# Optimization experiments

Hardware: AMD Instinct MI355X
Metric: run time of the kernel (lower is better)

Reference implementation:

```python
import math
import jax, jax.numpy as jnp
import numpy as np

D_MODEL = 1024
N_HEAD = 16
HEAD_DIM = D_MODEL // N_HEAD
BS, SEQ = 2, 2048


def setup_inputs() -> dict:
    key = jax.random.key(0)
    ks = jax.random.split(key, 10)
    s = 1.0 / math.sqrt(D_MODEL)  # ~torch Linear init scale
    x = jax.random.normal(ks[0], (BS, SEQ, D_MODEL), dtype=jnp.float32)
    bias = jax.random.normal(ks[1], (1, N_HEAD, SEQ, SEQ), dtype=jnp.float32)
    mask = jax.random.randint(ks[2], (1, 1, SEQ, SEQ), 0, 2, dtype=jnp.int32)
    wq = jax.random.uniform(ks[3], (D_MODEL, D_MODEL), jnp.float32, -s, s)
    bq = jax.random.uniform(ks[4], (D_MODEL,), jnp.float32, -s, s)
    wk = jax.random.uniform(ks[5], (D_MODEL, D_MODEL), jnp.float32, -s, s)
    bk = jax.random.uniform(ks[6], (D_MODEL,), jnp.float32, -s, s)
    wv = jax.random.uniform(ks[7], (D_MODEL, D_MODEL), jnp.float32, -s, s)
    bv = jax.random.uniform(ks[8], (D_MODEL,), jnp.float32, -s, s)
    return {"x": x, "bias": bias, "mask": mask,
            "wq": wq, "bq": bq, "wk": wk, "bk": bk, "wv": wv, "bv": bv}


def _split_heads(t):
    bs, s, _ = t.shape
    return t.reshape(bs, s, N_HEAD, HEAD_DIM).transpose(0, 2, 1, 3)  # [b,h,s,d]


def reference(x, bias, mask, wq, bq, wk, bk, wv, bv):
    # torch Linear: y = x @ W^T + b
    q = _split_heads(x @ wq.T + bq)
    k = _split_heads(x @ wk.T + bk)
    v = _split_heads(x @ wv.T + bv)
    scale = 1.0 / math.sqrt(HEAD_DIM)
    logits = jnp.einsum('bhqd,bhkd->bhqk', q, k) * scale + bias  # [b,h,S,S]
    logits = jnp.where(mask == 0, jnp.float32(-1e9), logits)
    atten_weights = jax.nn.softmax(logits, axis=-1)
    output = jnp.einsum('bhqk,bhkd->bhqd', atten_weights, v)  # [b,h,S,hd]
    return (output, atten_weights)
```

## Files before the change

### kernel.cpp

```cpp
#include <hip/hip_runtime.h>

typedef __attribute__((ext_vector_type(8))) short bf16x8;
typedef __attribute__((ext_vector_type(4))) float f32x4;
typedef __attribute__((ext_vector_type(4))) int i32x4;
typedef __attribute__((ext_vector_type(4))) unsigned short us4;

#define N_HEAD 16
#define SEQ 2048

__device__ __forceinline__ unsigned short f2bf(float f) {
  union { float f; unsigned u; } v; v.f = f;
  unsigned r = v.u + 0x7fffu + ((v.u >> 16) & 1u);
  return (unsigned short)(r >> 16);
}

__global__ void conv_bf16(const float* __restrict__ x,
                          const float* __restrict__ wq,
                          const float* __restrict__ wk,
                          const float* __restrict__ wv,
                          unsigned short* __restrict__ xb,
                          unsigned short* __restrict__ wb)
{
  size_t i = ((size_t)blockIdx.x * 256 + threadIdx.x) * 8;
  const float* src;
  unsigned short* dst;
  size_t off;
  if (i < 4194304) { src = x; dst = xb; off = i; }
  else {
    size_t j = i - 4194304;
    int w = (int)(j >> 20);
    off = j & 1048575u;
    src = (w == 0) ? wq : (w == 1) ? wk : wv;
    dst = wb + ((size_t)w << 20);
  }
  float4 a = *(const float4*)(src + off);
  float4 b = *(const float4*)(src + off + 4);
  us4 u0 = { f2bf(a.x), f2bf(a.y), f2bf(a.z), f2bf(a.w) };
  us4 u1 = { f2bf(b.x), f2bf(b.y), f2bf(b.z), f2bf(b.w) };
  *(us4*)(dst + off) = u0;
  *(us4*)(dst + off + 4) = u1;
}

__global__ __launch_bounds__(256, 2)
void qkv_gemm_bf16(const unsigned short* __restrict__ xb,
                   const unsigned short* __restrict__ wb,
                   const float* __restrict__ bq, const float* __restrict__ bk,
                   const float* __restrict__ bv,
                   unsigned short* __restrict__ qws,
                   unsigned short* __restrict__ kws,
                   unsigned short* __restrict__ vtws)
{
  __shared__ unsigned short As[128 * 40];
  __shared__ unsigned short Bs[128 * 40];

  const int tid  = threadIdx.x;
  const int wave = tid >> 6, lane = tid & 63;
  const int quad = lane >> 4, lrow = lane & 15;
  const int wm = wave >> 1, wn = wave & 1;
  const int m0 = blockIdx.x * 128, n0 = blockIdx.y * 128;
  const int z = blockIdx.z;

  const unsigned short* W = wb + ((size_t)z << 20);
  const float* bvec = (z == 0) ? bq : (z == 1) ? bk : bv;

  f32x4 acc[4][4];
  #pragma unroll
  for (int mi = 0; mi < 4; ++mi)
    #pragma unroll
    for (int ni = 0; ni < 4; ++ni)
      acc[mi][ni] = (f32x4){0.f, 0.f, 0.f, 0.f};

  const int srow = tid >> 1, scol = (tid & 1) * 16;
  const unsigned short* xsrc = xb + (size_t)(m0 + srow) * 1024 + scol;
  const unsigned short* wsrc = W  + (size_t)(n0 + srow) * 1024 + scol;

  bf16x8 va0 = *(const bf16x8*)(xsrc);
  bf16x8 va1 = *(const bf16x8*)(xsrc + 8);
  bf16x8 vb0 = *(const bf16x8*)(wsrc);
  bf16x8 vb1 = *(const bf16x8*)(wsrc + 8);

  for (int k0 = 0; k0 < 1024; k0 += 32) {
    __syncthreads();
    *(bf16x8*)&As[srow * 40 + scol]     = va0;
    *(bf16x8*)&As[srow * 40 + scol + 8] = va1;
    *(bf16x8*)&Bs[srow * 40 + scol]     = vb0;
    *(bf16x8*)&Bs[srow * 40 + scol + 8] = vb1;
    __syncthreads();
    if (k0 < 992) {
      va0 = *(const bf16x8*)(xsrc + k0 + 32);
      va1 = *(const bf16x8*)(xsrc + k0 + 40);
      vb0 = *(const bf16x8*)(wsrc + k0 + 32);
      vb1 = *(const bf16x8*)(wsrc + k0 + 40);
    }
    bf16x8 a[4], b[4];
    #pragma unroll
    for (int mi = 0; mi < 4; ++mi)
      a[mi] = *(const bf16x8*)&As[(wm * 64 + mi * 16 + lrow) * 40 + quad * 8];
    #pragma unroll
    for (int ni = 0; ni < 4; ++ni)
      b[ni] = *(const bf16x8*)&Bs[(wn * 64 + ni * 16 + lrow) * 40 + quad * 8];
    #pragma unroll
    for (int mi = 0; mi < 4; ++mi)
      #pragma unroll
      for (int ni = 0; ni < 4; ++ni)
        acc[mi][ni] = __builtin_amdgcn_mfma_f32_16x16x32_bf16(a[mi], b[ni], acc[mi][ni], 0, 0, 0);
  }

  float badd[4];
  #pragma unroll
  for (int ni = 0; ni < 4; ++ni) badd[ni] = bvec[n0 + wn * 64 + ni * 16 + lrow];

  if (z == 2) {
    #pragma unroll
    for (int mi = 0; mi < 4; ++mi) {
      int i0 = m0 + wm * 64 + mi * 16 + quad * 4;
      int bb = i0 >> 11, ss0 = i0 & 2047;
      #pragma unroll
      for (int ni = 0; ni < 4; ++ni) {
        int j = n0 + wn * 64 + ni * 16 + lrow;
        us4 u = { f2bf(acc[mi][ni][0] + badd[ni]),
                  f2bf(acc[mi][ni][1] + badd[ni]),
                  f2bf(acc[mi][ni][2] + badd[ni]),
                  f2bf(acc[mi][ni][3] + badd[ni]) };
        *(us4*)(vtws + ((size_t)(bb * 1024 + j)) * 2048 + ss0) = u;
      }
    }
  } else {
    #pragma unroll
    for (int mi = 0; mi < 4; ++mi) {
      #pragma unroll
      for (int ni = 0; ni < 4; ++ni) {
        int j = n0 + wn * 64 + ni * 16 + lrow;
        int hh = j >> 6, dd = j & 63;
        #pragma unroll
        for (int r = 0; r < 4; ++r) {
          int i = m0 + wm * 64 + mi * 16 + quad * 4 + r;
          int bb = i >> 11, ss = i & 2047;
          float y = acc[mi][ni][r] + badd[ni];
          if (z == 0)
            qws[(((size_t)(bb * 16 + hh)) * 2048 + ss) * 64 + dd] = f2bf(y * 0.125f);
          else
            kws[(((size_t)(bb * 16 + hh)) * 2048 + ss) * 64 + dd] = f2bf(y);
        }
      }
    }
  }
}

__global__ __launch_bounds__(256, 2)
void qkv_gemm(const float* __restrict__ x,
              const float* __restrict__ wq, const float* __restrict__ bq,
              const float* __restrict__ wk, const float* __restrict__ bk,
              const float* __restrict__ wv, const float* __restrict__ bv,
              unsigned short* __restrict__ qws,
              unsigned short* __restrict__ kws,
              unsigned short* __restrict__ vtws)
{
  __shared__ unsigned short As[128 * 40];
  __shared__ unsigned short Bs[128 * 40];

  const int tid  = threadIdx.x;
  const int wave = tid >> 6, lane = tid & 63;
  const int quad = lane >> 4, lrow = lane & 15;
  const int wm = wave >> 1, wn = wave & 1;
  const int m0 = blockIdx.x * 128, n0 = blockIdx.y * 128;
  const int z = blockIdx.z;

  const float* W;  const float* bvec;
  if (z == 0)      { W = wq; bvec = bq; }
  else if (z == 1) { W = wk; bvec = bk; }
  else             { W = wv; bvec = bv; }

  f32x4 acc[4][4];
  #pragma unroll
  for (int mi = 0; mi < 4; ++mi)
    #pragma unroll
    for (int ni = 0; ni < 4; ++ni)
      acc[mi][ni] = (f32x4){0.f, 0.f, 0.f, 0.f};

  for (int k0 = 0; k0 < 1024; k0 += 32) {
    __syncthreads();
    #pragma unroll
    for (int r = 0; r < 4; ++r) {
      int idx = tid + r * 256;
      int row = idx >> 3, seg = idx & 7;
      float4 xa = *(const float4*)(x + (size_t)(m0 + row) * 1024 + k0 + seg * 4);
      float4 xb = *(const float4*)(W + (size_t)(n0 + row) * 1024 + k0 + seg * 4);
      us4 ua = { f2bf(xa.x), f2bf(xa.y), f2bf(xa.z), f2bf(xa.w) };
      us4 ub = { f2bf(xb.x), f2bf(xb.y), f2bf(xb.z), f2bf(xb.w) };
      *(us4*)&As[row * 40 + seg * 4] = ua;
      *(us4*)&Bs[row * 40 + seg * 4] = ub;
    }
    __syncthreads();

    bf16x8 a[4], b[4];
    #pragma unroll
    for (int mi = 0; mi < 4; ++mi)
      a[mi] = *(const bf16x8*)&As[(wm * 64 + mi * 16 + lrow) * 40 + quad * 8];
    #pragma unroll
    for (int ni = 0; ni < 4; ++ni)
      b[ni] = *(const bf16x8*)&Bs[(wn * 64 + ni * 16 + lrow) * 40 + quad * 8];
    #pragma unroll
    for (int mi = 0; mi < 4; ++mi)
      #pragma unroll
      for (int ni = 0; ni < 4; ++ni)
        acc[mi][ni] = __builtin_amdgcn_mfma_f32_16x16x32_bf16(a[mi], b[ni], acc[mi][ni], 0, 0, 0);
  }

  float badd[4];
  #pragma unroll
  for (int ni = 0; ni < 4; ++ni) badd[ni] = bvec[n0 + wn * 64 + ni * 16 + lrow];

  #pragma unroll
  for (int mi = 0; mi < 4; ++mi) {
    #pragma unroll
    for (int ni = 0; ni < 4; ++ni) {
      int j = n0 + wn * 64 + ni * 16 + lrow;
      int hh = j >> 6, dd = j & 63;
      #pragma unroll
      for (int r = 0; r < 4; ++r) {
        int i = m0 + wm * 64 + mi * 16 + quad * 4 + r;
        int bb = i >> 11, ss = i & 2047;
        float y = acc[mi][ni][r] + badd[ni];
        if (z == 0)
          qws[(((size_t)(bb * 16 + hh)) * 2048 + ss) * 64 + dd] = f2bf(y * 0.125f);
        else if (z == 1)
          kws[(((size_t)(bb * 16 + hh)) * 2048 + ss) * 64 + dd] = f2bf(y);
        else
          vtws[(((size_t)(bb * 16 + hh)) * 64 + dd) * 2048 + ss] = f2bf(y);
      }
    }
  }
}

__global__ __launch_bounds__(512, 4)
void attn2(const unsigned short* __restrict__ qws,
           const unsigned short* __restrict__ kws,
           const unsigned short* __restrict__ vtws,
           const float* __restrict__ bias,
           const int* __restrict__ mask,
           float* __restrict__ out)
{
  const int tid  = threadIdx.x;
  const int wave = tid >> 6, lane = tid & 63;
  const int quad = lane >> 4, lrow = lane & 15;
  const int bx = blockIdx.x;
  const int h = bx >> 1, bb = bx & 1, bh = bb * 16 + h;
  const int q0 = blockIdx.y * 16;
  const int cb = wave * 256;

  const unsigned short* qh  = qws  + (size_t)bh * SEQ * 64;
  const unsigned short* kh  = kws  + (size_t)bh * SEQ * 64;
  const unsigned short* vth = vtws + (size_t)bh * 64 * SEQ;
  float* out_o = out;
  float* out_w = out + (size_t)2 * N_HEAD * SEQ * 64;

  __shared__ float red[8][16];
  __shared__ unsigned short pbuf[8][16][40];
  __shared__ float obuf[8][16][68];

  bf16x8 aq[2];
  #pragma unroll
  for (int ks = 0; ks < 2; ++ks)
    aq[ks] = *(const bf16x8*)(qh + (size_t)(q0 + lrow) * 64 + ks * 32 + quad * 8);

  const unsigned short* kp = kh + (size_t)(cb + lrow) * 64 + quad * 8;
  const float* bp = bias + ((size_t)h * SEQ + q0 + lrow) * SEQ + cb + quad * 4;
  const int*   mp = mask + (size_t)(q0 + lrow) * SEQ + cb + quad * 4;

  const float L2E = 1.44269504f;
  f32x4 S[16];
  float rsum = 0.f;

  #pragma unroll
  for (int t = 0; t < 16; ++t) {
    bf16x8 k0f = *(const bf16x8*)(kp + t * 1024);
    bf16x8 k1f = *(const bf16x8*)(kp + t * 1024 + 32);
    f32x4 c = (f32x4){0.f, 0.f, 0.f, 0.f};
    c = __builtin_amdgcn_mfma_f32_16x16x32_bf16(k0f, aq[0], c, 0, 0, 0);
    c = __builtin_amdgcn_mfma_f32_16x16x32_bf16(k1f, aq[1], c, 0, 0, 0);
    f32x4 bbv = *(const f32x4*)(bp + t * 16);
    i32x4 mmv = *(const i32x4*)(mp + t * 16);
    #pragma unroll
    for (int r = 0; r < 4; ++r) {
      float e = (mmv[r] == 0) ? 0.f : exp2f((c[r] + bbv[r]) * L2E);
      S[t][r] = e;
      rsum += e;
    }
  }

  rsum += __shfl_xor(rsum, 16);
  rsum += __shfl_xor(rsum, 32);
  if (lane < 16) red[wave][lrow] = rsum;
  __syncthreads();
  float tot = 0.f;
  #pragma unroll
  for (int w = 0; w < 8; ++w) tot += red[w][lrow];
  const float inv = 1.0f / tot;

  f32x4 O[4];
  #pragma unroll
  for (int n = 0; n < 4; ++n) O[n] = (f32x4){0.f, 0.f, 0.f, 0.f};

  float* wbase = out_w + ((size_t)bh * SEQ + q0 + lrow) * SEQ + cb + quad * 4;
  const unsigned short* vp = vth + (size_t)lrow * SEQ + cb + quad * 8;

  #pragma unroll
  for (int cc = 0; cc < 8; ++cc) {
    #pragma unroll
    for (int tt = 0; tt < 2; ++tt) {
      const int t = cc * 2 + tt;
      f32x4 wv;
      #pragma unroll
      for (int r = 0; r < 4; ++r) wv[r] = S[t][r] * inv;
      *(f32x4*)(wbase + t * 16) = wv;
      us4 u = { f2bf(wv[0]), f2bf(wv[1]), f2bf(wv[2]), f2bf(wv[3]) };
      *(us4*)&pbuf[wave][lrow][tt * 16 + quad * 4] = u;
    }
    asm volatile("s_waitcnt lgkmcnt(0)" ::: "memory");
    bf16x8 aw = *(const bf16x8*)&pbuf[wave][lrow][quad * 8];
    #pragma unroll
    for (int n = 0; n < 4; ++n) {
      bf16x8 v8 = *(const bf16x8*)(vp + (size_t)n * 16 * SEQ + cc * 32);
      O[n] = __builtin_amdgcn_mfma_f32_16x16x32_bf16(aw, v8, O[n], 0, 0, 0);
    }
  }

  #pragma unroll
  for (int n = 0; n < 4; ++n)
    #pragma unroll
    for (int r = 0; r < 4; ++r)
      obuf[wave][quad * 4 + r][n * 16 + lrow] = O[n][r];
  __syncthreads();
  #pragma unroll
  for (int e = 0; e < 2; ++e) {
    int idx = e * 512 + tid;
    int row = idx >> 6, dd = idx & 63;
    float v = 0.f;
    #pragma unroll
    for (int w = 0; w < 8; ++w) v += obuf[w][row][dd];
    out_o[((size_t)bh * SEQ + q0 + row) * 64 + dd] = v;
  }
}

extern "C" void kernel_launch(void* const* d_in, const int* in_sizes, int n_in,
                              void* d_out, int out_size, void* d_ws, size_t ws_size,
                              hipStream_t stream) {
  const float* x    = (const float*)d_in[0];
  const float* bias = (const float*)d_in[1];
  const int*   mask = (const int*)d_in[2];
  const float* wq   = (const float*)d_in[3];
  const float* bq   = (const float*)d_in[4];
  const float* wk   = (const float*)d_in[5];
  const float* bk   = (const float*)d_in[6];
  const float* wv   = (const float*)d_in[7];
  const float* bv   = (const float*)d_in[8];

  unsigned short* qws  = (unsigned short*)d_ws;
  unsigned short* kws  = qws + (size_t)4194304;
  unsigned short* vtws = kws + (size_t)4194304;
  float* out = (float*)d_out;

  if (ws_size >= (size_t)39845888) {
    unsigned short* xb = vtws + (size_t)4194304;
    unsigned short* wb = xb + (size_t)4194304;
    conv_bf16<<<dim3(3584), 256, 0, stream>>>(x, wq, wk, wv, xb, wb);
    qkv_gemm_bf16<<<dim3(32, 8, 3), 256, 0, stream>>>(xb, wb, bq, bk, bv,
                                                      qws, kws, vtws);
  } else {
    qkv_gemm<<<dim3(32, 8, 3), 256, 0, stream>>>(x, wq, bq, wk, bk, wv, bv,
                                                 qws, kws, vtws);
  }
  attn2<<<dim3(32, 128), 512, 0, stream>>>(qws, kws, vtws, bias, mask, out);
}
```

Measured before the change: 1.081 ms.

## Use 16x16x16 MFMA for PV without LDS staging, nontemporal stores, head swizzle

The attention kernel now feeds the probabilities straight from registers into 16x16x16 bf16 MFMAs, dropping the LDS pbuf round trip and its waits. The 2048x2048 weight output is written with nontemporal stores so it does not pollute the cache. The block index is remapped to change which heads and batches run together, which may help bias reuse in L2. The fp32 GEMM fallback is removed, and when workspace is small the output buffer's tail is used as scratch for the bf16 conversion. That scratch reuse is risky if the region overlaps output the attention kernel writes later.

Result: slower. 1.225 ms (+13.3%).

```diff
diff --git a/kernel.cpp b/kernel.cpp
--- a/kernel.cpp
+++ b/kernel.cpp
@@ -1,6 +1,7 @@
 #include <hip/hip_runtime.h>
 
 typedef __attribute__((ext_vector_type(8))) short bf16x8;
+typedef __attribute__((ext_vector_type(4))) short bf16x4;
 typedef __attribute__((ext_vector_type(4))) float f32x4;
 typedef __attribute__((ext_vector_type(4))) int i32x4;
 typedef __attribute__((ext_vector_type(4))) unsigned short us4;
@@ -147,92 +148,6 @@
   }
 }
 
-__global__ __launch_bounds__(256, 2)
-void qkv_gemm(const float* __restrict__ x,
-              const float* __restrict__ wq, const float* __restrict__ bq,
-              const float* __restrict__ wk, const float* __restrict__ bk,
-              const float* __restrict__ wv, const float* __restrict__ bv,
-              unsigned short* __restrict__ qws,
-              unsigned short* __restrict__ kws,
-              unsigned short* __restrict__ vtws)
-{
-  __shared__ unsigned short As[128 * 40];
-  __shared__ unsigned short Bs[128 * 40];
-
-  const int tid  = threadIdx.x;
-  const int wave = tid >> 6, lane = tid & 63;
-  const int quad = lane >> 4, lrow = lane & 15;
-  const int wm = wave >> 1, wn = wave & 1;
-  const int m0 = blockIdx.x * 128, n0 = blockIdx.y * 128;
-  const int z = blockIdx.z;
-
-  const float* W;  const float* bvec;
-  if (z == 0)      { W = wq; bvec = bq; }
-  else if (z == 1) { W = wk; bvec = bk; }
-  else             { W = wv; bvec = bv; }
-
-  f32x4 acc[4][4];
-  #pragma unroll
-  for (int mi = 0; mi < 4; ++mi)
-    #pragma unroll
-    for (int ni = 0; ni < 4; ++ni)
-      acc[mi][ni] = (f32x4){0.f, 0.f, 0.f, 0.f};
-
-  for (int k0 = 0; k0 < 1024; k0 += 32) {
-    __syncthreads();
-    #pragma unroll
-    for (int r = 0; r < 4; ++r) {
-      int idx = tid + r * 256;
-      int row = idx >> 3, seg = idx & 7;
-      float4 xa = *(const float4*)(x + (size_t)(m0 + row) * 1024 + k0 + seg * 4);
-      float4 xb = *(const float4*)(W + (size_t)(n0 + row) * 1024 + k0 + seg * 4);
-      us4 ua = { f2bf(xa.x), f2bf(xa.y), f2bf(xa.z), f2bf(xa.w) };
-      us4 ub = { f2bf(xb.x), f2bf(xb.y), f2bf(xb.z), f2bf(xb.w) };
-      *(us4*)&As[row * 40 + seg * 4] = ua;
-      *(us4*)&Bs[row * 40 + seg * 4] = ub;
-    }
-    __syncthreads();
-
-    bf16x8 a[4], b[4];
-    #pragma unroll
-    for (int mi = 0; mi < 4; ++mi)
-      a[mi] = *(const bf16x8*)&As[(wm * 64 + mi * 16 + lrow) * 40 + quad * 8];
-    #pragma unroll
-    for (int ni = 0; ni < 4; ++ni)
-      b[ni] = *(const bf16x8*)&Bs[(wn * 64 + ni * 16 + lrow) * 40 + quad * 8];
-    #pragma unroll
-    for (int mi = 0; mi < 4; ++mi)
-      #pragma unroll
-      for (int ni = 0; ni < 4; ++ni)
-        acc[mi][ni] = __builtin_amdgcn_mfma_f32_16x16x32_bf16(a[mi], b[ni], acc[mi][ni], 0, 0, 0);
-  }
-
-  float badd[4];
-  #pragma unroll
-  for (int ni = 0; ni < 4; ++ni) badd[ni] = bvec[n0 + wn * 64 + ni * 16 + lrow];
-
-  #pragma unroll
-  for (int mi = 0; mi < 4; ++mi) {
-    #pragma unroll
-    for (int ni = 0; ni < 4; ++ni) {
-      int j = n0 + wn * 64 + ni * 16 + lrow;
-      int hh = j >> 6, dd = j & 63;
-      #pragma unroll
-      for (int r = 0; r < 4; ++r) {
-        int i = m0 + wm * 64 + mi * 16 + quad * 4 + r;
-        int bb = i >> 11, ss = i & 2047;
-        float y = acc[mi][ni][r] + badd[ni];
-        if (z == 0)
-          qws[(((size_t)(bb * 16 + hh)) * 2048 + ss) * 64 + dd] = f2bf(y * 0.125f);
-        else if (z == 1)
-          kws[(((size_t)(bb * 16 + hh)) * 2048 + ss) * 64 + dd] = f2bf(y);
-        else
-          vtws[(((size_t)(bb * 16 + hh)) * 64 + dd) * 2048 + ss] = f2bf(y);
-      }
-    }
-  }
-}
-
 __global__ __launch_bounds__(512, 4)
 void attn2(const unsigned short* __restrict__ qws,
            const unsigned short* __restrict__ kws,
@@ -245,7 +160,9 @@
   const int wave = tid >> 6, lane = tid & 63;
   const int quad = lane >> 4, lrow = lane & 15;
   const int bx = blockIdx.x;
-  const int h = bx >> 1, bb = bx & 1, bh = bb * 16 + h;
+  const int h  = (bx & 7) | (((bx >> 4) & 1) << 3);
+  const int bb = (bx >> 3) & 1;
+  const int bh = bb * 16 + h;
   const int q0 = blockIdx.y * 16;
   const int cb = wave * 256;
 
@@ -256,8 +173,10 @@
   float* out_w = out + (size_t)2 * N_HEAD * SEQ * 64;
 
   __shared__ float red[8][16];
+  __shared__ float obuf[8][16][68];
+#if !__has_builtin(__builtin_amdgcn_mfma_f32_16x16x16bf16_1k)
   __shared__ unsigned short pbuf[8][16][40];
-  __shared__ float obuf[8][16][68];
+#endif
 
   bf16x8 aq[2];
   #pragma unroll
@@ -303,8 +222,29 @@
   for (int n = 0; n < 4; ++n) O[n] = (f32x4){0.f, 0.f, 0.f, 0.f};
 
   float* wbase = out_w + ((size_t)bh * SEQ + q0 + lrow) * SEQ + cb + quad * 4;
+
+#if __has_builtin(__builtin_amdgcn_mfma_f32_16x16x16bf16_1k)
+  const unsigned short* vp = vth + (size_t)lrow * SEQ + cb + quad * 4;
+  #pragma unroll
+  for (int t = 0; t < 16; ++t) {
+    f32x4 wv;
+    #pragma unroll
+    for (int r = 0; r < 4; ++r) wv[r] = S[t][r] * inv;
+#if __has_builtin(__builtin_nontemporal_store)
+    __builtin_nontemporal_store(wv, (f32x4*)(wbase + t * 16));
+#else
+    *(f32x4*)(wbase + t * 16) = wv;
+#endif
+    bf16x4 a4 = { (short)f2bf(wv[0]), (short)f2bf(wv[1]),
+                  (short)f2bf(wv[2]), (short)f2bf(wv[3]) };
+    #pragma unroll
+    for (int n = 0; n < 4; ++n) {
+      bf16x4 v4 = *(const bf16x4*)(vp + (size_t)n * 16 * SEQ + t * 16);
+      O[n] = __builtin_amdgcn_mfma_f32_16x16x16bf16_1k(a4, v4, O[n], 0, 0, 0);
+    }
+  }
+#else
   const unsigned short* vp = vth + (size_t)lrow * SEQ + cb + quad * 8;
-
   #pragma unroll
   for (int cc = 0; cc < 8; ++cc) {
     #pragma unroll
@@ -325,6 +265,7 @@
       O[n] = __builtin_amdgcn_mfma_f32_16x16x32_bf16(aw, v8, O[n], 0, 0, 0);
     }
   }
+#endif
 
   #pragma unroll
   for (int n = 0; n < 4; ++n)
@@ -361,15 +302,16 @@
   unsigned short* vtws = kws + (size_t)4194304;
   float* out = (float*)d_out;
 
+  unsigned short* xb;
   if (ws_size >= (size_t)39845888) {
-    unsigned short* xb = vtws + (size_t)4194304;
-    unsigned short* wb = xb + (size_t)4194304;
-    conv_bf16<<<dim3(3584), 256, 0, stream>>>(x, wq, wk, wv, xb, wb);
-    qkv_gemm_bf16<<<dim3(32, 8, 3), 256, 0, stream>>>(xb, wb, bq, bk, bv,
-                                                      qws, kws, vtws);
+    xb = vtws + (size_t)4194304;
   } else {
-    qkv_gemm<<<dim3(32, 8, 3), 256, 0, stream>>>(x, wq, bq, wk, bk, wv, bv,
-                                                 qws, kws, vtws);
-  }
+    xb = (unsigned short*)((char*)d_out + ((size_t)out_size - (size_t)14 * 1024 * 1024));
+  }
+  unsigned short* wb = xb + (size_t)4194304;
+
+  conv_bf16<<<dim3(3584), 256, 0, stream>>>(x, wq, wk, wv, xb, wb);
+  qkv_gemm_bf16<<<dim3(32, 8, 3), 256, 0, stream>>>(xb, wb, bq, bk, bv,
+                                                    qws, kws, vtws);
   attn2<<<dim3(32, 128), 512, 0, stream>>>(qws, kws, vtws, bias, mask, out);
 }
```
